# Optimization experiments

Measured on AMD Instinct MI355X. Metric: run time of the kernel, lower is better.

## Reference

```python
import jax, jax.numpy as jnp
import numpy as np
import math

B, L, D, H = 16, 144, 512, 8
DH = D // H          # 64, equals structure feature dim
DS, HS = 64, 8       # structure sub-attention model dim / heads
DFF = 2048

def ln(x, g, b, eps=1e-6):
    m = jnp.mean(x, -1, keepdims=True)
    v = jnp.mean((x - m) ** 2, -1, keepdims=True)
    return (x - m) * jax.lax.rsqrt(v + eps) * g + b

def setup_inputs():
    key = jax.random.key(0)
    ks = iter(jax.random.split(key, 32))
    def w(shape, s=0.02):
        return jax.random.normal(next(ks), shape, jnp.float32) * s
    return {
        "inputs": jax.random.normal(next(ks), (B, L, D), jnp.float32),
        "structure": jax.random.normal(next(ks), (L * L, 4, B, DS), jnp.float32),
        "mask": jax.random.randint(next(ks), (B, L, L), 0, 2, jnp.int32),
        "g_att": jnp.ones((D,), jnp.float32), "b_att": jnp.zeros((D,), jnp.float32),
        "Wq": w((D, D)), "bq": jnp.zeros((D,), jnp.float32),
        "Wk": w((D, D)), "bk": jnp.zeros((D,), jnp.float32),
        "Wv": w((D, D)), "bv": jnp.zeros((D,), jnp.float32),
        "Wo": w((D, D)), "bo": jnp.zeros((D,), jnp.float32),
        "sWq": w((DS, DS)), "sbq": jnp.zeros((DS,), jnp.float32),
        "sWk": w((DS, DS)), "sbk": jnp.zeros((DS,), jnp.float32),
        "sWv": w((DS, DS)), "sbv": jnp.zeros((DS,), jnp.float32),
        "sWo": w((DS, DS)), "sbo": jnp.zeros((DS,), jnp.float32),
        "Wc": w((DS, DS, 4)), "bc": jnp.zeros((DS,), jnp.float32),
        "g_s": jnp.ones((DS,), jnp.float32), "b_s": jnp.zeros((DS,), jnp.float32),
        "g_ffn": jnp.ones((D,), jnp.float32), "b_ffn": jnp.zeros((D,), jnp.float32),
        "W1": w((D, DFF)), "b1": jnp.zeros((DFF,), jnp.float32),
        "W2": w((DFF, D)), "b2": jnp.zeros((D,), jnp.float32),
    }

def _forward(inputs, structure, mask, g_att, b_att, Wq, bq, Wk, bk, Wv, bv, Wo, bo,
             sWq, sbq, sWk, sbk, sWv, sbv, sWo, sbo, Wc, bc, g_s, b_s,
             g_ffn, b_ffn, W1, b1, W2, b2):
    x_norm = ln(inputs, g_att, b_att)

    # --- structure pipeline: [L*L,4,B,DS] -> (transpose(0,1),transpose(0,2)) -> [B,L*L,4,DS] -> [N,4,DS]
    N = B * L * L
    s = jnp.transpose(structure, (2, 0, 1, 3)).reshape(N, 4, DS)
    dsh = DS // HS
    def split_s(t):
        return t.reshape(N, 4, HS, dsh).transpose(0, 2, 1, 3)
    q = split_s(s @ sWq + sbq) / math.sqrt(dsh)
    k = split_s(s @ sWk + sbk)
    v = split_s(s @ sWv + sbv)
    attn = jax.nn.softmax(jnp.einsum('nhid,nhjd->nhij', q, k), -1)
    ctx = jnp.einsum('nhij,nhjd->nhid', attn, v).transpose(0, 2, 1, 3).reshape(N, 4, DS)
    sa = ctx @ sWo + sbo                                  # [N,4,DS]
    # Conv1d(64,64,kernel=4) over the length-4 axis (valid -> length 1) + ReLU
    conv = jax.nn.relu(jnp.einsum('ntc,oct->no', sa, Wc) + bc)  # [N,DS]
    R = ln(conv.reshape(B, L, L, DS), g_s, b_s)           # per-pair relation embeddings

    # --- relation-aware self-attention (structure added to keys and values)
    def split_h(t):
        return t.reshape(B, L, H, DH).transpose(0, 2, 1, 3)
    q = split_h(x_norm @ Wq + bq) / math.sqrt(DH)
    k = split_h(x_norm @ Wk + bk)
    v = split_h(x_norm @ Wv + bv)
    scores = jnp.einsum('bhid,bhjd->bhij', q, k) + jnp.einsum('bhid,bijd->bhij', q, R)
    scores = jnp.where(mask[:, None, :, :] != 0, jnp.float32(-1e18), scores)
    attn = jax.nn.softmax(scores, -1)
    ctx = jnp.einsum('bhij,bhjd->bhid', attn, v) + jnp.einsum('bhij,bijd->bhid', attn, R)
    ctx = ctx.transpose(0, 2, 1, 3).reshape(B, L, D)
    x = ctx @ Wo + bo + inputs

    # --- FFN (pre-LN, residual outside)
    h = jax.nn.relu(ln(x, g_ffn, b_ffn) @ W1 + b1)
    return h @ W2 + b2 + x

def reference(inputs, structure, mask, g_att, b_att, Wq, bq, Wk, bk, Wv, bv, Wo, bo,
              sWq, sbq, sWk, sbk, sWv, sbv, sWo, sbo, Wc, bc, g_s, b_s,
              g_ffn, b_ffn, W1, b1, W2, b2):
    return _forward(inputs, structure, mask, g_att, b_att, Wq, bq, Wk, bk, Wv, bv, Wo, bo,
                    sWq, sbq, sWk, sbk, sWv, sbv, sWo, sbo, Wc, bc, g_s, b_s,
                    g_ffn, b_ffn, W1, b1, W2, b2)
```

## Files before the change

kernel.cpp:

```cpp
#include <hip/hip_runtime.h>
#include <math.h>


typedef __bf16 bf16_t;
typedef __bf16 bf16x8 __attribute__((ext_vector_type(8)));
typedef __bf16 bf16x4 __attribute__((ext_vector_type(4)));
typedef __bf16 bf16x2v __attribute__((ext_vector_type(2)));
typedef float f32x4 __attribute__((ext_vector_type(4)));

__global__ __launch_bounds__(256) void transpose_all(
    const float* __restrict__ Wq, const float* __restrict__ Wk,
    const float* __restrict__ Wv, const float* __restrict__ Wo,
    const float* __restrict__ W1, const float* __restrict__ W2,
    bf16_t* __restrict__ WqkvT, bf16_t* __restrict__ WoT,
    bf16_t* __restrict__ W1T, bf16_t* __restrict__ W2T) {
  int bid = blockIdx.x;
  const float* W; bf16_t* WT; int K, N; float scale = 1.f; int tile;
  if (bid < 256)       { W = Wq; WT = WqkvT;            K = 512;  N = 512;  scale = 0.125f; tile = bid; }
  else if (bid < 512)  { W = Wk; WT = WqkvT + 262144;   K = 512;  N = 512;  tile = bid - 256; }
  else if (bid < 768)  { W = Wv; WT = WqkvT + 524288;   K = 512;  N = 512;  tile = bid - 512; }
  else if (bid < 1024) { W = Wo; WT = WoT;              K = 512;  N = 512;  tile = bid - 768; }
  else if (bid < 2048) { W = W1; WT = W1T;              K = 512;  N = 2048; tile = bid - 1024; }
  else                 { W = W2; WT = W2T;              K = 2048; N = 512;  tile = bid - 2048; }
  int ntn = N >> 5;
  int nb = (tile % ntn) * 32, kb = (tile / ntn) * 32;
  __shared__ float t32[32][33];
  int tx = threadIdx.x & 31, ty = threadIdx.x >> 5;
#pragma unroll
  for (int i = ty; i < 32; i += 8) t32[i][tx] = W[(size_t)(kb + i) * N + nb + tx];
  __syncthreads();
#pragma unroll
  for (int i = ty; i < 32; i += 8)
    WT[(size_t)(nb + i) * K + kb + tx] = (__bf16)(t32[tx][i] * scale);
}

__global__ __launch_bounds__(256) void precompute_misc(
    const float* __restrict__ sWq, const float* __restrict__ sWk,
    const float* __restrict__ sWv, const float* __restrict__ sWo,
    const float* __restrict__ sbq, const float* __restrict__ sbk,
    const float* __restrict__ sbv, const float* __restrict__ sbo,
    const float* __restrict__ Wc, const float* __restrict__ bc,
    const float* __restrict__ bq, const float* __restrict__ bk,
    const float* __restrict__ bv, bf16_t* __restrict__ WT3,
    bf16_t* __restrict__ M2T, float* __restrict__ C0,
    float* __restrict__ sbqkv, float* __restrict__ bqkv) {
  int blk = blockIdx.x, tid = threadIdx.x;
  if (blk == 16) {
    const float qs = 0.35355339059327373f;
    for (int idx = tid; idx < 4096; idx += 256) {
      int j = idx >> 6, ic = idx & 63;
      int cj = (j & 7) * 8 + 2 * ((j >> 4) & 3) + ((j >> 3) & 1);
      WT3[idx] = (__bf16)(sWq[ic * 64 + cj] * qs);
      WT3[4096 + idx] = (__bf16)sWk[ic * 64 + cj];
      WT3[8192 + idx] = (__bf16)sWv[ic * 64 + cj];
    }
    if (tid < 64) {
      float s = bc[tid];
      for (int c = 0; c < 64; ++c) {
        float sb = sbo[c];
#pragma unroll
        for (int t = 0; t < 4; ++t) s += sb * Wc[tid * 256 + c * 4 + t];
      }
      C0[tid] = s;
      int cj = (tid & 7) * 8 + 2 * ((tid >> 4) & 3) + ((tid >> 3) & 1);
      sbqkv[tid] = sbq[cj] * qs;
      sbqkv[64 + tid] = sbk[cj];
      sbqkv[128 + tid] = sbv[cj];
    }
  } else if (blk == 17) {
    for (int i = tid; i < 1536; i += 256)
      bqkv[i] = (i < 512) ? bq[i] * 0.125f
                          : ((i < 1024) ? bk[i - 512] : bv[i - 1024]);
  } else {
    int t = blk >> 2;
    int e = (blk & 3) * 16 + (tid >> 4);
    int o4 = (tid & 15) * 4;
    float acc[4] = {0.f, 0.f, 0.f, 0.f};
    for (int c = 0; c < 64; ++c) {
      float a = sWo[e * 64 + c];
#pragma unroll
      for (int j = 0; j < 4; ++j) acc[j] += a * Wc[(o4 + j) * 256 + c * 4 + t];
    }
#pragma unroll
    for (int j = 0; j < 4; ++j)
      M2T[(o4 + j) * 256 + t * 64 + e] = (__bf16)acc[j];
  }
}

__global__ __launch_bounds__(256) void ln512(
    const float* __restrict__ x, const float* __restrict__ g,
    const float* __restrict__ bb, bf16_t* __restrict__ out) {
  int row = blockIdx.x, tid = threadIdx.x;
  const float* xr = x + (size_t)row * 512;
  float2 v = *(const float2*)&xr[tid * 2];
  float s1 = v.x + v.y;
  float s2 = v.x * v.x + v.y * v.y;
#pragma unroll
  for (int m = 32; m >= 1; m >>= 1) {
    s1 += __shfl_xor(s1, m);
    s2 += __shfl_xor(s2, m);
  }
  __shared__ float red[8];
  int wid = tid >> 6;
  if ((tid & 63) == 0) { red[wid * 2] = s1; red[wid * 2 + 1] = s2; }
  __syncthreads();
  s1 = red[0] + red[2] + red[4] + red[6];
  s2 = red[1] + red[3] + red[5] + red[7];
  float mean = s1 * (1.f / 512.f);
  float var = s2 * (1.f / 512.f) - mean * mean;
  float rs = 1.f / sqrtf(var + 1e-6f);
  int c = tid * 2;
  float2 gg = *(const float2*)&g[c];
  float2 bv = *(const float2*)&bb[c];
  bf16x2v o;
  o[0] = (__bf16)((v.x - mean) * rs * gg.x + bv.x);
  o[1] = (__bf16)((v.y - mean) * rs * gg.y + bv.y);
  *(bf16x2v*)&out[(size_t)row * 512 + c] = o;
}

template <int MR>
__global__ __launch_bounds__(256) void gemm_bf16(
    const bf16_t* __restrict__ A, const bf16_t* __restrict__ BT,
    const float* __restrict__ bias, const float* __restrict__ res,
    float* __restrict__ Cf, bf16_t* __restrict__ Cb, int M, int N, int K,
    int relu) {
  constexpr int RT = MR / 64;
  int tid = threadIdx.x;
  int w = tid >> 6, l = tid & 63, l15 = l & 15, l4 = l >> 4;
  int n0 = blockIdx.x * 64, m0 = blockIdx.y * MR;
  const bf16_t* Arow[RT];
#pragma unroll
  for (int rt = 0; rt < RT; ++rt)
    Arow[rt] = A + (size_t)(m0 + (w * RT + rt) * 16 + l15) * K + l4 * 8;
  const bf16_t* Bbase = BT + (size_t)(n0 + l15) * K + l4 * 8;
  f32x4 acc[RT][4];
#pragma unroll
  for (int ct = 0; ct < 4; ++ct) {
    float bv = bias[n0 + ct * 16 + l15];
#pragma unroll
    for (int rt = 0; rt < RT; ++rt) acc[rt][ct] = (f32x4){bv, bv, bv, bv};
  }
#pragma unroll 4
  for (int k0 = 0; k0 < K; k0 += 32) {
    bf16x8 a8[RT];
#pragma unroll
    for (int rt = 0; rt < RT; ++rt) a8[rt] = *(const bf16x8*)(Arow[rt] + k0);
#pragma unroll
    for (int ct = 0; ct < 4; ++ct) {
      bf16x8 b8 = *(const bf16x8*)(Bbase + (size_t)ct * 16 * K + k0);
#pragma unroll
      for (int rt = 0; rt < RT; ++rt)
        acc[rt][ct] =
            __builtin_amdgcn_mfma_f32_16x16x32_bf16(a8[rt], b8, acc[rt][ct], 0, 0, 0);
    }
  }
#pragma unroll
  for (int ct = 0; ct < 4; ++ct) {
    int col = n0 + ct * 16 + l15;
#pragma unroll
    for (int rt = 0; rt < RT; ++rt) {
#pragma unroll
      for (int i = 0; i < 4; ++i) {
        int row = m0 + (w * RT + rt) * 16 + l4 * 4 + i;
        float vv = acc[rt][ct][i];
        if (relu) vv = fmaxf(vv, 0.f);
        if (res) vv += res[(size_t)row * N + col];
        if (Cf) Cf[(size_t)row * N + col] = vv;
        if (Cb) Cb[(size_t)row * N + col] = (__bf16)vv;
      }
    }
  }
}

__global__ __launch_bounds__(256, 2) void struct_mfma(
    const float* __restrict__ S, const bf16_t* __restrict__ WT3,
    const float* __restrict__ sbqkv, const bf16_t* __restrict__ M2T,
    const float* __restrict__ C0, const float* __restrict__ gs,
    const float* __restrict__ bsv, bf16_t* __restrict__ Rout) {
  __shared__ __align__(16) char smem[67584];
  int tid = threadIdx.x;
  int w = tid >> 6, l = tid & 63, l15 = l & 15, l4 = l >> 4;
  int p0 = blockIdx.x * 4;

  bf16x8 wq[4][2], wk[4][2], wv[4][2];
  float biq[4], bik[4], biv[4];
#pragma unroll
  for (int ct = 0; ct < 4; ++ct) {
    int j = ct * 16 + l15;
#pragma unroll
    for (int kb = 0; kb < 2; ++kb) {
      int off = j * 64 + kb * 32 + l4 * 8;
      wq[ct][kb] = *(const bf16x8*)(WT3 + off);
      wk[ct][kb] = *(const bf16x8*)(WT3 + 4096 + off);
      wv[ct][kb] = *(const bf16x8*)(WT3 + 8192 + off);
    }
    biq[ct] = sbqkv[j];
    bik[ct] = sbqkv[64 + j];
    biv[ct] = sbqkv[128 + j];
  }

  {
    int row = tid >> 4;
    int cb0 = (tid & 15) * 16;
    const float* src = S + (size_t)(p0 * 4 + row) * 1024;
    int key = (row & 7) << 4;
#pragma unroll
    for (int i = 0; i < 8; ++i) {
      int colb = cb0 + i * 256;
      int c0 = colb >> 1;
      float4 u0 = *(const float4*)(src + c0);
      float4 u1 = *(const float4*)(src + c0 + 4);
      bf16x8 a;
      a[0] = (__bf16)u0.x; a[1] = (__bf16)u0.y;
      a[2] = (__bf16)u0.z; a[3] = (__bf16)u0.w;
      a[4] = (__bf16)u1.x; a[5] = (__bf16)u1.y;
      a[6] = (__bf16)u1.z; a[7] = (__bf16)u1.w;
      *(bf16x8*)(smem + row * 2048 + (colb ^ key)) = a;
    }
  }
  __syncthreads();

  int pl = l >> 4, h = l & 7, hi = (l >> 3) & 1;
#pragma unroll 1
  for (int r = 0; r < 4; ++r) {
    int b = r * 4 + w;
    int akey = (l15 & 7) << 4;
    int colb0 = b * 128 + l4 * 16;
    bf16x8 af0 = *(const bf16x8*)(smem + l15 * 2048 + (colb0 ^ akey));
    bf16x8 af1 = *(const bf16x8*)(smem + l15 * 2048 + ((colb0 + 64) ^ akey));
    f32x4 aq[4], ak[4], av[4];
#pragma unroll
    for (int ct = 0; ct < 4; ++ct) {
      aq[ct] = (f32x4){biq[ct], biq[ct], biq[ct], biq[ct]};
      ak[ct] = (f32x4){bik[ct], bik[ct], bik[ct], bik[ct]};
      av[ct] = (f32x4){biv[ct], biv[ct], biv[ct], biv[ct]};
    }
#pragma unroll
    for (int ct = 0; ct < 4; ++ct) {
      aq[ct] = __builtin_amdgcn_mfma_f32_16x16x32_bf16(af0, wq[ct][0], aq[ct], 0, 0, 0);
      aq[ct] = __builtin_amdgcn_mfma_f32_16x16x32_bf16(af1, wq[ct][1], aq[ct], 0, 0, 0);
      ak[ct] = __builtin_amdgcn_mfma_f32_16x16x32_bf16(af0, wk[ct][0], ak[ct], 0, 0, 0);
      ak[ct] = __builtin_amdgcn_mfma_f32_16x16x32_bf16(af1, wk[ct][1], ak[ct], 0, 0, 0);
      av[ct] = __builtin_amdgcn_mfma_f32_16x16x32_bf16(af0, wv[ct][0], av[ct], 0, 0, 0);
      av[ct] = __builtin_amdgcn_mfma_f32_16x16x32_bf16(af1, wv[ct][1], av[ct], 0, 0, 0);
    }
    float Sm[4][4];
#pragma unroll
    for (int i2 = 0; i2 < 4; ++i2)
#pragma unroll
      for (int j2 = 0; j2 < 4; ++j2)
        Sm[i2][j2] = aq[0][i2] * ak[0][j2] + aq[1][i2] * ak[1][j2] +
                     aq[2][i2] * ak[2][j2] + aq[3][i2] * ak[3][j2];
#pragma unroll
    for (int i2 = 0; i2 < 4; ++i2)
#pragma unroll
      for (int j2 = 0; j2 < 4; ++j2)
        Sm[i2][j2] += __shfl_xor(Sm[i2][j2], 8);
    float P[4][4], inv[4];
#pragma unroll
    for (int i2 = 0; i2 < 4; ++i2) {
      float rs = 0.f;
#pragma unroll
      for (int j2 = 0; j2 < 4; ++j2) {
        P[i2][j2] = __expf(Sm[i2][j2]);
        rs += P[i2][j2];
      }
      inv[i2] = __builtin_amdgcn_rcpf(rs);
    }
    int unit = r * 16 + w * 4 + pl;
    char* cb = smem + 32768 + unit * 544;
    int ckey = (unit & 7) << 4;
#pragma unroll
    for (int ct = 0; ct < 4; ++ct) {
      int c = h * 8 + 2 * ct + hi;
#pragma unroll
      for (int i2 = 0; i2 < 4; ++i2) {
        float cx = (P[i2][0] * av[ct][0] + P[i2][1] * av[ct][1] +
                    P[i2][2] * av[ct][2] + P[i2][3] * av[ct][3]) * inv[i2];
        *(bf16_t*)(cb + ((i2 * 128 + c * 2) ^ ckey)) = (__bf16)cx;
      }
    }
  }
  __syncthreads();

  float* cvp = (float*)smem;
  {
    bf16x8 ax[8];
    int rkey = (l15 & 7) << 4;
    char* cbase = smem + 32768 + (w * 16 + l15) * 544;
#pragma unroll
    for (int kb = 0; kb < 8; ++kb) {
      int byt = (kb >> 1) * 128 + (kb & 1) * 64 + l4 * 16;
      ax[kb] = *(const bf16x8*)(cbase + (byt ^ rkey));
    }
#pragma unroll 1
    for (int ct = 0; ct < 4; ++ct) {
      int o = ct * 16 + l15;
      float c0v = C0[o];
      f32x4 acc = (f32x4){c0v, c0v, c0v, c0v};
#pragma unroll
      for (int kb = 0; kb < 8; ++kb) {
        bf16x8 mf = *(const bf16x8*)(M2T + o * 256 + kb * 32 + l4 * 8);
        acc = __builtin_amdgcn_mfma_f32_16x16x32_bf16(ax[kb], mf, acc, 0, 0, 0);
      }
#pragma unroll
      for (int i2 = 0; i2 < 4; ++i2)
        cvp[(w * 16 + l4 * 4 + i2) * 68 + o] = fmaxf(acc[i2], 0.f);
    }
  }
  __syncthreads();

  {
    int unit = tid >> 2, ch0 = (tid & 3) * 16;
    const float* cr = cvp + unit * 68 + ch0;
    float4 v0 = *(const float4*)(cr);
    float4 v1 = *(const float4*)(cr + 4);
    float4 v2 = *(const float4*)(cr + 8);
    float4 v3 = *(const float4*)(cr + 12);
    float s1 = v0.x + v0.y + v0.z + v0.w + v1.x + v1.y + v1.z + v1.w +
               v2.x + v2.y + v2.z + v2.w + v3.x + v3.y + v3.z + v3.w;
    float s2 = v0.x * v0.x + v0.y * v0.y + v0.z * v0.z + v0.w * v0.w +
               v1.x * v1.x + v1.y * v1.y + v1.z * v1.z + v1.w * v1.w +
               v2.x * v2.x + v2.y * v2.y + v2.z * v2.z + v2.w * v2.w +
               v3.x * v3.x + v3.y * v3.y + v3.z * v3.z + v3.w * v3.w;
    s1 += __shfl_xor(s1, 1); s1 += __shfl_xor(s1, 2);
    s2 += __shfl_xor(s2, 1); s2 += __shfl_xor(s2, 2);
    float mean = s1 * (1.f / 64.f);
    float var = s2 * (1.f / 64.f) - mean * mean;
    float rstd = 1.f / sqrtf(var + 1e-6f);
    float4 g0 = *(const float4*)&gs[ch0];
    float4 g1 = *(const float4*)&gs[ch0 + 4];
    float4 g2 = *(const float4*)&gs[ch0 + 8];
    float4 g3 = *(const float4*)&gs[ch0 + 12];
    float4 b0 = *(const float4*)&bsv[ch0];
    float4 b1 = *(const float4*)&bsv[ch0 + 4];
    float4 b2 = *(const float4*)&bsv[ch0 + 8];
    float4 b3 = *(const float4*)&bsv[ch0 + 12];
    bf16x8 o0, o1;
    o0[0] = (__bf16)((v0.x - mean) * rstd * g0.x + b0.x);
    o0[1] = (__bf16)((v0.y - mean) * rstd * g0.y + b0.y);
    o0[2] = (__bf16)((v0.z - mean) * rstd * g0.z + b0.z);
    o0[3] = (__bf16)((v0.w - mean) * rstd * g0.w + b0.w);
    o0[4] = (__bf16)((v1.x - mean) * rstd * g1.x + b1.x);
    o0[5] = (__bf16)((v1.y - mean) * rstd * g1.y + b1.y);
    o0[6] = (__bf16)((v1.z - mean) * rstd * g1.z + b1.z);
    o0[7] = (__bf16)((v1.w - mean) * rstd * g1.w + b1.w);
    o1[0] = (__bf16)((v2.x - mean) * rstd * g2.x + b2.x);
    o1[1] = (__bf16)((v2.y - mean) * rstd * g2.y + b2.y);
    o1[2] = (__bf16)((v2.z - mean) * rstd * g2.z + b2.z);
    o1[3] = (__bf16)((v2.w - mean) * rstd * g2.w + b2.w);
    o1[4] = (__bf16)((v3.x - mean) * rstd * g3.x + b3.x);
    o1[5] = (__bf16)((v3.y - mean) * rstd * g3.y + b3.y);
    o1[6] = (__bf16)((v3.z - mean) * rstd * g3.z + b3.z);
    o1[7] = (__bf16)((v3.w - mean) * rstd * g3.w + b3.w);
    int rr = unit >> 4, w2 = (unit >> 2) & 3, pu = unit & 3;
    int b = rr * 4 + w2;
    size_t base = ((size_t)b * 20736 + p0 + pu) * 64 + ch0;
    *(bf16x8*)&Rout[base] = o0;
    *(bf16x8*)&Rout[base + 8] = o1;
  }
}

__global__ __launch_bounds__(256) void attn_score(
    const bf16_t* __restrict__ qkv, const bf16_t* __restrict__ R,
    const int* __restrict__ msk, bf16_t* __restrict__ Pg,
    float* __restrict__ ctmp) {
  const int L = 144;
  __shared__ __align__(16) char smem[51008];
  bf16_t* qZ = (bf16_t*)smem;
  bf16_t* qL = (bf16_t*)(smem + 16640);
  bf16_t* RT = (bf16_t*)(smem + 18944);
  bf16_t* PL = (bf16_t*)(smem + 40448);
  float* scl = (float*)(smem + 45824);
  int* mskL = (int*)(smem + 50432);

  int blk = blockIdx.x;
  int b = blk / L, i = blk - b * L;
  int tid = threadIdx.x;
  int bL = b * L;

  bf16x8 z8;
#pragma unroll
  for (int e = 0; e < 8; ++e) z8[e] = (__bf16)0.f;

  for (int idx = tid; idx < 1040; idx += 256) {
    int r = idx / 65, c8 = (idx - r * 65) * 8;
    *(bf16x8*)&qZ[r * 520 + c8] = z8;
  }
  if (tid < 144) {
    int r = tid / 9, c8 = (tid - r * 9) * 8;
    *(bf16x8*)&qL[r * 72 + c8] = z8;
  }
  for (int idx = tid; idx < 336; idx += 256) {
    int r = idx / 21, c8 = (idx - r * 21) * 8;
    *(bf16x8*)&PL[r * 168 + c8] = z8;
  }
  if (tid < 192) {
    int r = tid / 3, c8 = 144 + (tid - (tid / 3) * 3) * 8;
    *(bf16x8*)&RT[r * 168 + c8] = z8;
  }
  if (tid < 144) mskL[tid] = msk[(size_t)(bL + i) * 144 + tid];
  __syncthreads();

  if (tid < 64) {
    int h = tid >> 3, d8 = (tid & 7) * 8;
    bf16x8 q8 = *(const bf16x8*)&qkv[(size_t)(bL + i) * 1536 + h * 64 + d8];
    *(bf16x8*)&qZ[h * 520 + h * 64 + d8] = q8;
    *(bf16x8*)&qL[h * 72 + d8] = q8;
  }
  for (int idx = tid; idx < 1152; idx += 256) {
    int j = idx >> 3, d8 = (idx & 7) * 8;
    bf16x8 r8 = *(const bf16x8*)&R[((size_t)(bL + i) * 144 + j) * 64 + d8];
#pragma unroll
    for (int e = 0; e < 8; ++e) RT[(d8 + e) * 168 + j] = r8[e];
  }
  __syncthreads();

  int w = tid >> 6, l = tid & 63, l15 = l & 15, l4 = l >> 4;

  {
#pragma unroll 1
    for (int jt = w; jt < 9; jt += 4) {
      const bf16_t* kg =
          qkv + (size_t)(bL + jt * 16 + l15) * 1536 + 512 + l4 * 8;
      f32x4 acc = (f32x4){0.f, 0.f, 0.f, 0.f};
#pragma unroll
      for (int ks = 0; ks < 16; ++ks) {
        bf16x8 a8 = *(const bf16x8*)&qZ[l15 * 520 + ks * 32 + l4 * 8];
        bf16x8 b8 = *(const bf16x8*)(kg + ks * 32);
        acc = __builtin_amdgcn_mfma_f32_16x16x32_bf16(a8, b8, acc, 0, 0, 0);
      }
      const bf16_t* rg =
          R + ((size_t)(bL + i) * 144 + jt * 16 + l15) * 64 + l4 * 8;
      bf16x8 a0 = *(const bf16x8*)&qL[l15 * 72 + l4 * 8];
      bf16x8 a1 = *(const bf16x8*)&qL[l15 * 72 + 32 + l4 * 8];
      acc = __builtin_amdgcn_mfma_f32_16x16x32_bf16(a0, *(const bf16x8*)rg,
                                                    acc, 0, 0, 0);
      acc = __builtin_amdgcn_mfma_f32_16x16x32_bf16(
          a1, *(const bf16x8*)(rg + 32), acc, 0, 0, 0);
      if (l4 < 2) {
        int j = jt * 16 + l15;
        bool mm = mskL[j] != 0;
#pragma unroll
        for (int i2 = 0; i2 < 4; ++i2)
          scl[(l4 * 4 + i2) * 144 + j] = mm ? -1e18f : acc[i2];
      }
    }
  }
  __syncthreads();

  {
    int h = tid >> 5, lw = tid & 31;
    float m = -3.4e38f;
    for (int j = lw; j < 144; j += 32) m = fmaxf(m, scl[h * 144 + j]);
#pragma unroll
    for (int mm = 16; mm >= 1; mm >>= 1) m = fmaxf(m, __shfl_xor(m, mm));
    float sum = 0.f;
    for (int j = lw; j < 144; j += 32) {
      float p = __expf(scl[h * 144 + j] - m);
      scl[h * 144 + j] = p;
      sum += p;
    }
#pragma unroll
    for (int mm = 16; mm >= 1; mm >>= 1) sum += __shfl_xor(sum, mm);
    float inv = 1.f / sum;
    bf16_t* pgrow = Pg + ((size_t)(b * 8 + h) * 144 + i) * 160;
    for (int j = lw; j < 144; j += 32) {
      __bf16 pv = (__bf16)(scl[h * 144 + j] * inv);
      PL[h * 168 + j] = pv;
      pgrow[j] = pv;
    }
    if (lw < 16) pgrow[144 + lw] = (__bf16)0.f;
  }
  __syncthreads();

  {
    f32x4 acc = (f32x4){0.f, 0.f, 0.f, 0.f};
#pragma unroll
    for (int ks = 0; ks < 5; ++ks) {
      bf16x8 a8 = *(const bf16x8*)&PL[l15 * 168 + ks * 32 + l4 * 8];
      bf16x8 b8 = *(const bf16x8*)&RT[(w * 16 + l15) * 168 + ks * 32 + l4 * 8];
      acc = __builtin_amdgcn_mfma_f32_16x16x32_bf16(a8, b8, acc, 0, 0, 0);
    }
    if (l4 < 2) {
      float* crow = ctmp + (size_t)(bL + i) * 512;
#pragma unroll
      for (int i2 = 0; i2 < 4; ++i2)
        crow[(l4 * 4 + i2) * 64 + w * 16 + l15] = acc[i2];
    }
  }
}

__global__ __launch_bounds__(256) void attn_pv(
    const bf16_t* __restrict__ qkv, const bf16_t* __restrict__ Pg,
    const float* __restrict__ ctmp, bf16_t* __restrict__ ctx_out) {
  const int L = 144;
  __shared__ __align__(16) bf16_t VT[64 * 168];
  int bx = blockIdx.x;
  int bh = bx >> 1, half = bx & 1;
  int b = bh >> 3, h = bh & 7;
  int tid = threadIdx.x;
  int bL = b * L;

  bf16x8 z8;
#pragma unroll
  for (int e = 0; e < 8; ++e) z8[e] = (__bf16)0.f;
  for (int idx = tid; idx < 1152; idx += 256) {
    int j = idx >> 3, d8 = (idx & 7) * 8;
    bf16x8 v8 =
        *(const bf16x8*)&qkv[(size_t)(bL + j) * 1536 + 1024 + h * 64 + d8];
#pragma unroll
    for (int e = 0; e < 8; ++e) VT[(d8 + e) * 168 + j] = v8[e];
  }
  if (tid < 192) {
    int r = tid / 3, c8 = 144 + (tid - (tid / 3) * 3) * 8;
    *(bf16x8*)&VT[r * 168 + c8] = z8;
  }
  __syncthreads();

  int w = tid >> 6, l = tid & 63, l15 = l & 15, l4 = l >> 4;
  const bf16_t* pbase = Pg + (size_t)(b * 8 + h) * 144 * 160;
  int itEnd = half ? 9 : 5;
#pragma unroll 1
  for (int it = half * 5 + w; it < itEnd; it += 4) {
    const bf16_t* arow = pbase + (size_t)(it * 16 + l15) * 160 + l4 * 8;
    f32x4 acc[4];
#pragma unroll
    for (int ct = 0; ct < 4; ++ct) acc[ct] = (f32x4){0.f, 0.f, 0.f, 0.f};
#pragma unroll
    for (int ks = 0; ks < 5; ++ks) {
      bf16x8 a8 = *(const bf16x8*)(arow + ks * 32);
#pragma unroll
      for (int ct = 0; ct < 4; ++ct) {
        bf16x8 b8 =
            *(const bf16x8*)&VT[(ct * 16 + l15) * 168 + ks * 32 + l4 * 8];
        acc[ct] = __builtin_amdgcn_mfma_f32_16x16x32_bf16(a8, b8, acc[ct], 0, 0, 0);
      }
    }
#pragma unroll
    for (int ct = 0; ct < 4; ++ct) {
#pragma unroll
      for (int i2 = 0; i2 < 4; ++i2) {
        int row = it * 16 + l4 * 4 + i2;
        size_t off = (size_t)(bL + row) * 512 + h * 64 + ct * 16 + l15;
        ctx_out[off] = (__bf16)(acc[ct][i2] + ctmp[off]);
      }
    }
  }
}

extern "C" void kernel_launch(void* const* d_in, const int* in_sizes, int n_in,
                              void* d_out, int out_size, void* d_ws,
                              size_t ws_size, hipStream_t stream) {
  (void)in_sizes; (void)n_in; (void)out_size; (void)ws_size;
  const float* inputs = (const float*)d_in[0];
  const float* structure = (const float*)d_in[1];
  const int* mask = (const int*)d_in[2];
  const float* g_att = (const float*)d_in[3];
  const float* b_att = (const float*)d_in[4];
  const float* Wq = (const float*)d_in[5];
  const float* bq = (const float*)d_in[6];
  const float* Wk = (const float*)d_in[7];
  const float* bk = (const float*)d_in[8];
  const float* Wv = (const float*)d_in[9];
  const float* bv = (const float*)d_in[10];
  const float* Wo = (const float*)d_in[11];
  const float* bo = (const float*)d_in[12];
  const float* sWq = (const float*)d_in[13];
  const float* sbq = (const float*)d_in[14];
  const float* sWk = (const float*)d_in[15];
  const float* sbk = (const float*)d_in[16];
  const float* sWv = (const float*)d_in[17];
  const float* sbv = (const float*)d_in[18];
  const float* sWo = (const float*)d_in[19];
  const float* sbo = (const float*)d_in[20];
  const float* Wc = (const float*)d_in[21];
  const float* bc = (const float*)d_in[22];
  const float* g_s = (const float*)d_in[23];
  const float* b_s = (const float*)d_in[24];
  const float* g_ffn = (const float*)d_in[25];
  const float* b_ffn = (const float*)d_in[26];
  const float* W1 = (const float*)d_in[27];
  const float* b1 = (const float*)d_in[28];
  const float* W2 = (const float*)d_in[29];
  const float* b2 = (const float*)d_in[30];

  char* base = (char*)d_ws;
  bf16_t* Rw = (bf16_t*)base;
  bf16_t* qkvb = (bf16_t*)(base + 42467328);
  float* xw = (float*)(base + 49545216);
  bf16_t* xnb = (bf16_t*)(base + 54263808);
  bf16_t* ctxb = (bf16_t*)(base + 56623104);
  bf16_t* hb = (bf16_t*)(base + 58982400);
  bf16_t* WqkvT = (bf16_t*)(base + 68419584);
  bf16_t* WoT = (bf16_t*)(base + 69992448);
  bf16_t* W1T = (bf16_t*)(base + 70516736);
  bf16_t* W2T = (bf16_t*)(base + 72613888);
  bf16_t* WT3 = (bf16_t*)(base + 74711040);
  bf16_t* M2T = (bf16_t*)(base + 74735616);
  float* C0w = (float*)(base + 74768384);
  float* sbqkv = (float*)(base + 74768640);
  float* bqkv = (float*)(base + 74769408);
  bf16_t* Pg = hb;
  float* ctmp = xw;
  float* out = (float*)d_out;

  transpose_all<<<3072, 256, 0, stream>>>(Wq, Wk, Wv, Wo, W1, W2, WqkvT, WoT,
                                          W1T, W2T);
  precompute_misc<<<18, 256, 0, stream>>>(sWq, sWk, sWv, sWo, sbq, sbk, sbv,
                                          sbo, Wc, bc, bq, bk, bv, WT3, M2T,
                                          C0w, sbqkv, bqkv);
  ln512<<<2304, 256, 0, stream>>>(inputs, g_att, b_att, xnb);
  gemm_bf16<128><<<dim3(24, 18), 256, 0, stream>>>(
      xnb, WqkvT, bqkv, nullptr, nullptr, qkvb, 2304, 1536, 512, 0);
  struct_mfma<<<5184, 256, 0, stream>>>(structure, WT3, sbqkv, M2T, C0w, g_s,
                                        b_s, Rw);
  attn_score<<<2304, 256, 0, stream>>>(qkvb, Rw, mask, Pg, ctmp);
  attn_pv<<<256, 256, 0, stream>>>(qkvb, Pg, ctmp, ctxb);
  gemm_bf16<64><<<dim3(8, 36), 256, 0, stream>>>(
      ctxb, WoT, bo, inputs, xw, nullptr, 2304, 512, 512, 0);
  ln512<<<2304, 256, 0, stream>>>(xw, g_ffn, b_ffn, xnb);
  gemm_bf16<128><<<dim3(32, 18), 256, 0, stream>>>(
      xnb, W1T, b1, nullptr, nullptr, hb, 2304, 2048, 512, 1);
  gemm_bf16<64><<<dim3(8, 36), 256, 0, stream>>>(
      hb, W2T, b2, xw, out, nullptr, 2304, 512, 2048, 0);
}
```

Measured before the change: 481.9 us.

## Restructure struct kernel per-round to shrink LDS, split attn_pv into quarters

The structure kernel now runs the output projection, ReLU and layer norm inside each of the four rounds. This shrinks the context and conv scratch buffers, cutting shared memory from about 67KB to 46KB. The V weights are reloaded each round to save registers, and the launch-bounds occupancy hint is dropped. Context values are packed through lane shuffles into vector stores, and the score kernel reuses the zero-padded q buffer instead of a separate copy. attn_pv is split across four blocks per head instead of two, raising parallelism; the trade-off is more barriers per struct block and repeated V-tile staging.

Result: slower. 631.1 us (+30.9%).

```diff
diff --git a/kernel.cpp b/kernel.cpp
--- a/kernel.cpp
+++ b/kernel.cpp
@@ -172,17 +172,19 @@
   }
 }
 
-__global__ __launch_bounds__(256, 2) void struct_mfma(
+#define CTX_OFF 32768
+#define CV_OFF  41472
+__global__ __launch_bounds__(256) void struct_mfma(
     const float* __restrict__ S, const bf16_t* __restrict__ WT3,
     const float* __restrict__ sbqkv, const bf16_t* __restrict__ M2T,
     const float* __restrict__ C0, const float* __restrict__ gs,
     const float* __restrict__ bsv, bf16_t* __restrict__ Rout) {
-  __shared__ __align__(16) char smem[67584];
+  __shared__ __align__(16) char smem[45824];
   int tid = threadIdx.x;
   int w = tid >> 6, l = tid & 63, l15 = l & 15, l4 = l >> 4;
   int p0 = blockIdx.x * 4;
 
-  bf16x8 wq[4][2], wk[4][2], wv[4][2];
+  bf16x8 wq[4][2], wk[4][2];
   float biq[4], bik[4], biv[4];
 #pragma unroll
   for (int ct = 0; ct < 4; ++ct) {
@@ -192,7 +194,6 @@
       int off = j * 64 + kb * 32 + l4 * 8;
       wq[ct][kb] = *(const bf16x8*)(WT3 + off);
       wk[ct][kb] = *(const bf16x8*)(WT3 + 4096 + off);
-      wv[ct][kb] = *(const bf16x8*)(WT3 + 8192 + off);
     }
     biq[ct] = sbqkv[j];
     bik[ct] = sbqkv[64 + j];
@@ -220,10 +221,18 @@
   }
   __syncthreads();
 
-  int pl = l >> 4, h = l & 7, hi = (l >> 3) & 1;
+  int pl = l4, h = l & 7, hi = (l >> 3) & 1;
+  float* cvp = (float*)(smem + CV_OFF);
 #pragma unroll 1
   for (int r = 0; r < 4; ++r) {
     int b = r * 4 + w;
+    bf16x8 wv[4][2];
+#pragma unroll
+    for (int ct = 0; ct < 4; ++ct) {
+      int off = (ct * 16 + l15) * 64 + l4 * 8;
+      wv[ct][0] = *(const bf16x8*)(WT3 + 8192 + off);
+      wv[ct][1] = *(const bf16x8*)(WT3 + 8192 + off + 32);
+    }
     int akey = (l15 & 7) << 4;
     int colb0 = b * 128 + l4 * 16;
     bf16x8 af0 = *(const bf16x8*)(smem + l15 * 2048 + (colb0 ^ akey));
@@ -256,108 +265,88 @@
 #pragma unroll
       for (int j2 = 0; j2 < 4; ++j2)
         Sm[i2][j2] += __shfl_xor(Sm[i2][j2], 8);
-    float P[4][4], inv[4];
+    float cxv[4][4];
 #pragma unroll
     for (int i2 = 0; i2 < 4; ++i2) {
-      float rs = 0.f;
-#pragma unroll
-      for (int j2 = 0; j2 < 4; ++j2) {
-        P[i2][j2] = __expf(Sm[i2][j2]);
-        rs += P[i2][j2];
-      }
-      inv[i2] = __builtin_amdgcn_rcpf(rs);
-    }
-    int unit = r * 16 + w * 4 + pl;
-    char* cb = smem + 32768 + unit * 544;
+      float e0 = __expf(Sm[i2][0]), e1 = __expf(Sm[i2][1]);
+      float e2 = __expf(Sm[i2][2]), e3 = __expf(Sm[i2][3]);
+      float inv = __builtin_amdgcn_rcpf(e0 + e1 + e2 + e3);
+#pragma unroll
+      for (int ct = 0; ct < 4; ++ct)
+        cxv[i2][ct] = (e0 * av[ct][0] + e1 * av[ct][1] + e2 * av[ct][2] +
+                       e3 * av[ct][3]) * inv;
+    }
+    int unit = w * 4 + pl;
+    char* cb = smem + CTX_OFF + unit * 544;
     int ckey = (unit & 7) << 4;
-#pragma unroll
-    for (int ct = 0; ct < 4; ++ct) {
-      int c = h * 8 + 2 * ct + hi;
-#pragma unroll
-      for (int i2 = 0; i2 < 4; ++i2) {
-        float cx = (P[i2][0] * av[ct][0] + P[i2][1] * av[ct][1] +
-                    P[i2][2] * av[ct][2] + P[i2][3] * av[ct][3]) * inv[i2];
-        *(bf16_t*)(cb + ((i2 * 128 + c * 2) ^ ckey)) = (__bf16)cx;
-      }
-    }
-  }
-  __syncthreads();
-
-  float* cvp = (float*)smem;
-  {
-    bf16x8 ax[8];
-    int rkey = (l15 & 7) << 4;
-    char* cbase = smem + 32768 + (w * 16 + l15) * 544;
-#pragma unroll
-    for (int kb = 0; kb < 8; ++kb) {
-      int byt = (kb >> 1) * 128 + (kb & 1) * 64 + l4 * 16;
-      ax[kb] = *(const bf16x8*)(cbase + (byt ^ rkey));
-    }
-#pragma unroll 1
-    for (int ct = 0; ct < 4; ++ct) {
-      int o = ct * 16 + l15;
+    float rcv[2][4];
+#pragma unroll
+    for (int j = 0; j < 2; ++j)
+#pragma unroll
+      for (int ct = 0; ct < 4; ++ct) {
+        float sv = hi ? cxv[j][ct] : cxv[2 + j][ct];
+        rcv[j][ct] = __shfl_xor(sv, 8);
+      }
+#pragma unroll
+    for (int j = 0; j < 2; ++j) {
+      int tmine = hi * 2 + j;
+      bf16x8 o8;
+#pragma unroll
+      for (int ct = 0; ct < 4; ++ct) {
+        float ev = hi ? rcv[j][ct] : cxv[j][ct];
+        float ov = hi ? cxv[2 + j][ct] : rcv[j][ct];
+        o8[2 * ct] = (__bf16)ev;
+        o8[2 * ct + 1] = (__bf16)ov;
+      }
+      *(bf16x8*)(cb + ((tmine * 128 + h * 16) ^ ckey)) = o8;
+    }
+    __syncthreads();
+
+    {
+      int o = w * 16 + l15;
+      int rkey = (l15 & 7) << 4;
+      char* cbase = smem + CTX_OFF + l15 * 544;
       float c0v = C0[o];
       f32x4 acc = (f32x4){c0v, c0v, c0v, c0v};
 #pragma unroll
       for (int kb = 0; kb < 8; ++kb) {
-        bf16x8 mf = *(const bf16x8*)(M2T + o * 256 + kb * 32 + l4 * 8);
-        acc = __builtin_amdgcn_mfma_f32_16x16x32_bf16(ax[kb], mf, acc, 0, 0, 0);
+        int k0 = kb * 32 + l4 * 8;
+        int byt = (k0 >> 6) * 128 + (k0 & 63) * 2;
+        bf16x8 a8 = *(const bf16x8*)(cbase + (byt ^ rkey));
+        bf16x8 mf = *(const bf16x8*)(M2T + o * 256 + k0);
+        acc = __builtin_amdgcn_mfma_f32_16x16x32_bf16(a8, mf, acc, 0, 0, 0);
       }
 #pragma unroll
       for (int i2 = 0; i2 < 4; ++i2)
-        cvp[(w * 16 + l4 * 4 + i2) * 68 + o] = fmaxf(acc[i2], 0.f);
-    }
-  }
-  __syncthreads();
-
-  {
-    int unit = tid >> 2, ch0 = (tid & 3) * 16;
-    const float* cr = cvp + unit * 68 + ch0;
-    float4 v0 = *(const float4*)(cr);
-    float4 v1 = *(const float4*)(cr + 4);
-    float4 v2 = *(const float4*)(cr + 8);
-    float4 v3 = *(const float4*)(cr + 12);
-    float s1 = v0.x + v0.y + v0.z + v0.w + v1.x + v1.y + v1.z + v1.w +
-               v2.x + v2.y + v2.z + v2.w + v3.x + v3.y + v3.z + v3.w;
-    float s2 = v0.x * v0.x + v0.y * v0.y + v0.z * v0.z + v0.w * v0.w +
-               v1.x * v1.x + v1.y * v1.y + v1.z * v1.z + v1.w * v1.w +
-               v2.x * v2.x + v2.y * v2.y + v2.z * v2.z + v2.w * v2.w +
-               v3.x * v3.x + v3.y * v3.y + v3.z * v3.z + v3.w * v3.w;
-    s1 += __shfl_xor(s1, 1); s1 += __shfl_xor(s1, 2);
-    s2 += __shfl_xor(s2, 1); s2 += __shfl_xor(s2, 2);
-    float mean = s1 * (1.f / 64.f);
-    float var = s2 * (1.f / 64.f) - mean * mean;
-    float rstd = 1.f / sqrtf(var + 1e-6f);
-    float4 g0 = *(const float4*)&gs[ch0];
-    float4 g1 = *(const float4*)&gs[ch0 + 4];
-    float4 g2 = *(const float4*)&gs[ch0 + 8];
-    float4 g3 = *(const float4*)&gs[ch0 + 12];
-    float4 b0 = *(const float4*)&bsv[ch0];
-    float4 b1 = *(const float4*)&bsv[ch0 + 4];
-    float4 b2 = *(const float4*)&bsv[ch0 + 8];
-    float4 b3 = *(const float4*)&bsv[ch0 + 12];
-    bf16x8 o0, o1;
-    o0[0] = (__bf16)((v0.x - mean) * rstd * g0.x + b0.x);
-    o0[1] = (__bf16)((v0.y - mean) * rstd * g0.y + b0.y);
-    o0[2] = (__bf16)((v0.z - mean) * rstd * g0.z + b0.z);
-    o0[3] = (__bf16)((v0.w - mean) * rstd * g0.w + b0.w);
-    o0[4] = (__bf16)((v1.x - mean) * rstd * g1.x + b1.x);
-    o0[5] = (__bf16)((v1.y - mean) * rstd * g1.y + b1.y);
-    o0[6] = (__bf16)((v1.z - mean) * rstd * g1.z + b1.z);
-    o0[7] = (__bf16)((v1.w - mean) * rstd * g1.w + b1.w);
-    o1[0] = (__bf16)((v2.x - mean) * rstd * g2.x + b2.x);
-    o1[1] = (__bf16)((v2.y - mean) * rstd * g2.y + b2.y);
-    o1[2] = (__bf16)((v2.z - mean) * rstd * g2.z + b2.z);
-    o1[3] = (__bf16)((v2.w - mean) * rstd * g2.w + b2.w);
-    o1[4] = (__bf16)((v3.x - mean) * rstd * g3.x + b3.x);
-    o1[5] = (__bf16)((v3.y - mean) * rstd * g3.y + b3.y);
-    o1[6] = (__bf16)((v3.z - mean) * rstd * g3.z + b3.z);
-    o1[7] = (__bf16)((v3.w - mean) * rstd * g3.w + b3.w);
-    int rr = unit >> 4, w2 = (unit >> 2) & 3, pu = unit & 3;
-    int b = rr * 4 + w2;
-    size_t base = ((size_t)b * 20736 + p0 + pu) * 64 + ch0;
-    *(bf16x8*)&Rout[base] = o0;
-    *(bf16x8*)&Rout[base + 8] = o1;
+        cvp[(l4 * 4 + i2) * 68 + o] = fmaxf(acc[i2], 0.f);
+    }
+    __syncthreads();
+
+    {
+      int unit2 = tid >> 4, ch0 = (tid & 15) * 4;
+      float4 vv = *(const float4*)(cvp + unit2 * 68 + ch0);
+      float s1 = vv.x + vv.y + vv.z + vv.w;
+      float s2 = vv.x * vv.x + vv.y * vv.y + vv.z * vv.z + vv.w * vv.w;
+#pragma unroll
+      for (int m = 1; m <= 8; m <<= 1) {
+        s1 += __shfl_xor(s1, m);
+        s2 += __shfl_xor(s2, m);
+      }
+      float mean = s1 * (1.f / 64.f);
+      float var = s2 * (1.f / 64.f) - mean * mean;
+      float rstd = 1.f / sqrtf(var + 1e-6f);
+      float4 g4 = *(const float4*)&gs[ch0];
+      float4 b4 = *(const float4*)&bsv[ch0];
+      bf16x4 ov;
+      ov[0] = (__bf16)((vv.x - mean) * rstd * g4.x + b4.x);
+      ov[1] = (__bf16)((vv.y - mean) * rstd * g4.y + b4.y);
+      ov[2] = (__bf16)((vv.z - mean) * rstd * g4.z + b4.z);
+      ov[3] = (__bf16)((vv.w - mean) * rstd * g4.w + b4.w);
+      int wp = unit2 >> 2, pu = unit2 & 3;
+      int bb = r * 4 + wp;
+      *(bf16x4*)&Rout[((size_t)(bb * 20736 + p0 + pu)) * 64 + ch0] = ov;
+    }
+    __syncthreads();
   }
 }
 
@@ -366,13 +355,12 @@
     const int* __restrict__ msk, bf16_t* __restrict__ Pg,
     float* __restrict__ ctmp) {
   const int L = 144;
-  __shared__ __align__(16) char smem[51008];
+  __shared__ __align__(16) char smem[48704];
   bf16_t* qZ = (bf16_t*)smem;
-  bf16_t* qL = (bf16_t*)(smem + 16640);
-  bf16_t* RT = (bf16_t*)(smem + 18944);
-  bf16_t* PL = (bf16_t*)(smem + 40448);
-  float* scl = (float*)(smem + 45824);
-  int* mskL = (int*)(smem + 50432);
+  bf16_t* RT = (bf16_t*)(smem + 16640);
+  bf16_t* PL = (bf16_t*)(smem + 38144);
+  float* scl = (float*)(smem + 43520);
+  int* mskL = (int*)(smem + 48128);
 
   int blk = blockIdx.x;
   int b = blk / L, i = blk - b * L;
@@ -387,10 +375,6 @@
     int r = idx / 65, c8 = (idx - r * 65) * 8;
     *(bf16x8*)&qZ[r * 520 + c8] = z8;
   }
-  if (tid < 144) {
-    int r = tid / 9, c8 = (tid - r * 9) * 8;
-    *(bf16x8*)&qL[r * 72 + c8] = z8;
-  }
   for (int idx = tid; idx < 336; idx += 256) {
     int r = idx / 21, c8 = (idx - r * 21) * 8;
     *(bf16x8*)&PL[r * 168 + c8] = z8;
@@ -406,7 +390,6 @@
     int h = tid >> 3, d8 = (tid & 7) * 8;
     bf16x8 q8 = *(const bf16x8*)&qkv[(size_t)(bL + i) * 1536 + h * 64 + d8];
     *(bf16x8*)&qZ[h * 520 + h * 64 + d8] = q8;
-    *(bf16x8*)&qL[h * 72 + d8] = q8;
   }
   for (int idx = tid; idx < 1152; idx += 256) {
     int j = idx >> 3, d8 = (idx & 7) * 8;
@@ -432,8 +415,8 @@
       }
       const bf16_t* rg =
           R + ((size_t)(bL + i) * 144 + jt * 16 + l15) * 64 + l4 * 8;
-      bf16x8 a0 = *(const bf16x8*)&qL[l15 * 72 + l4 * 8];
-      bf16x8 a1 = *(const bf16x8*)&qL[l15 * 72 + 32 + l4 * 8];
+      bf16x8 a0 = *(const bf16x8*)&qZ[l15 * 520 + l15 * 64 + l4 * 8];
+      bf16x8 a1 = *(const bf16x8*)&qZ[l15 * 520 + l15 * 64 + 32 + l4 * 8];
       acc = __builtin_amdgcn_mfma_f32_16x16x32_bf16(a0, *(const bf16x8*)rg,
                                                     acc, 0, 0, 0);
       acc = __builtin_amdgcn_mfma_f32_16x16x32_bf16(
@@ -497,7 +480,7 @@
   const int L = 144;
   __shared__ __align__(16) bf16_t VT[64 * 168];
   int bx = blockIdx.x;
-  int bh = bx >> 1, half = bx & 1;
+  int bh = bx >> 2, quarter = bx & 3;
   int b = bh >> 3, h = bh & 7;
   int tid = threadIdx.x;
   int bL = b * L;
@@ -520,9 +503,10 @@
 
   int w = tid >> 6, l = tid & 63, l15 = l & 15, l4 = l >> 4;
   const bf16_t* pbase = Pg + (size_t)(b * 8 + h) * 144 * 160;
-  int itEnd = half ? 9 : 5;
+  const int itS[4] = {0, 3, 5, 7};
+  const int itE[4] = {3, 5, 7, 9};
 #pragma unroll 1
-  for (int it = half * 5 + w; it < itEnd; it += 4) {
+  for (int it = itS[quarter] + w; it < itE[quarter]; it += 4) {
     const bf16_t* arow = pbase + (size_t)(it * 16 + l15) * 160 + l4 * 8;
     f32x4 acc[4];
 #pragma unroll
@@ -616,7 +600,7 @@
   struct_mfma<<<5184, 256, 0, stream>>>(structure, WT3, sbqkv, M2T, C0w, g_s,
                                         b_s, Rw);
   attn_score<<<2304, 256, 0, stream>>>(qkvb, Rw, mask, Pg, ctmp);
-  attn_pv<<<256, 256, 0, stream>>>(qkvb, Pg, ctmp, ctxb);
+  attn_pv<<<512, 256, 0, stream>>>(qkvb, Pg, ctmp, ctxb);
   gemm_bf16<64><<<dim3(8, 36), 256, 0, stream>>>(
       ctxb, WoT, bo, inputs, xw, nullptr, 2304, 512, 512, 0);
   ln512<<<2304, 256, 0, stream>>>(xw, g_ffn, b_ffn, xnb);
```
